# Optimization experiments

Measured on AMD Instinct MI355X. Metric: run time of the kernel, lower is better.

The kernel has to match this reference:

```python
import jax, jax.numpy as jnp
import numpy as np

# irreps: node in/out = 32x0e + 16x1o (dim 80), sh = 1x0e + 1x1o (dim 4)
N_NODES, N_EDGES = 8000, 64000
NUM_BASIS, RAD_HIDDEN = 8, 64
WEIGHT_NUMEL = 2304  # 32*32 + 32*16 + 16*16 + 16*32
EPS = 1e-8
INV_SQRT3 = 1.0 / np.sqrt(3.0)
# e3nn path weights (normalization='component', path_normalization='element'):
# into 0e outputs: sqrt(ir.dim=1 / (32+16)); into 1o outputs: sqrt(3 / (32+16))
PW0 = float(np.sqrt(1.0 / 48.0))
PW1 = float(np.sqrt(3.0 / 48.0))


def setup_inputs() -> dict:
    key = jax.random.key(0)
    ks = jax.random.split(key, 10)
    node_features = jax.random.normal(ks[0], (N_NODES, 80), dtype=jnp.float32)
    edge_index = jax.random.randint(ks[1], (2, N_EDGES), 0, N_NODES, dtype=jnp.int64)
    edge_sh = jax.random.normal(ks[2], (N_EDGES, 4), dtype=jnp.float32)
    edge_radial_emb = jax.random.uniform(ks[3], (N_EDGES, NUM_BASIS), dtype=jnp.float32)
    # RadialMLP params (Linear 8->64, SiLU, Linear 64->2304)
    rW1 = jax.random.normal(ks[4], (NUM_BASIS, RAD_HIDDEN), dtype=jnp.float32) / np.sqrt(NUM_BASIS)
    rb1 = jnp.zeros((RAD_HIDDEN,), dtype=jnp.float32)
    rW2 = jax.random.normal(ks[5], (RAD_HIDDEN, WEIGHT_NUMEL), dtype=jnp.float32) / np.sqrt(RAD_HIDDEN)
    rb2 = jnp.zeros((WEIGHT_NUMEL,), dtype=jnp.float32)
    # o3.Linear weights (per-irrep mixing matrices, e3nn init ~ N(0,1))
    Wl0 = jax.random.normal(ks[6], (32, 32), dtype=jnp.float32)
    Wl1 = jax.random.normal(ks[7], (16, 16), dtype=jnp.float32)
    return {"node_features": node_features, "edge_index": edge_index,
            "edge_sh": edge_sh, "edge_radial_emb": edge_radial_emb,
            "rW1": rW1, "rb1": rb1, "rW2": rW2, "rb2": rb2,
            "Wl0": Wl0, "Wl1": Wl1}


def reference(node_features, edge_index, edge_sh, edge_radial_emb,
              rW1, rb1, rW2, rb2, Wl0, Wl1):
    N = node_features.shape[0]
    src, dst = edge_index[0], edge_index[1]
    # radial MLP -> per-edge tensor-product weights [E, 2304] (fp32 path)
    h = jax.nn.silu(edge_radial_emb @ rW1 + rb1)
    tpw = h @ rW2 + rb2
    E = tpw.shape[0]
    wA = tpw[:, :1024].reshape(E, 32, 32)      # 0e x 0e -> 0e
    wB = tpw[:, 1024:1536].reshape(E, 32, 16)  # 0e x 1o -> 1o
    wC = tpw[:, 1536:1792].reshape(E, 16, 16)  # 1o x 0e -> 1o
    wD = tpw[:, 1792:2304].reshape(E, 16, 32)  # 1o x 1o -> 0e
    # gather source node features
    xs = node_features[src, :32]                       # [E,32] scalars
    xv = node_features[src, 32:].reshape(E, 16, 3)     # [E,16,3] vectors
    sh0 = edge_sh[:, 0]                                # [E]
    shv = edge_sh[:, 1:4]                              # [E,3]
    # equivariant tensor product messages
    dotv = jnp.einsum('euk,ek->eu', xv, shv)           # 1o.1o -> 0e
    msg_s = PW0 * (jnp.einsum('euw,eu->ew', wA, xs * sh0[:, None])
                   + INV_SQRT3 * jnp.einsum('euw,eu->eu' if False else 'euw,eu->ew', wD, dotv))
    msg_v = (PW1 * INV_SQRT3) * (jnp.einsum('euw,eu,ek->ewk', wB, xs, shv)
                                 + jnp.einsum('euw,euk->ewk', wC, xv) * sh0[:, None, None])
    messages = jnp.concatenate([msg_s, msg_v.reshape(E, 48)], axis=-1)  # [E,80]
    # scatter-sum aggregation over destination nodes
    agg = jax.ops.segment_sum(messages, dst, num_segments=N)            # [N,80]
    # equivariant linear (per-irrep mixing, fan-in normalized)
    lin_s = (agg[:, :32] @ Wl0) / np.sqrt(32.0)
    lin_v = jnp.einsum('nuk,uv->nvk', agg[:, 32:].reshape(N, 16, 3), Wl1) / np.sqrt(16.0)
    # SafeNormActivation: silu on scalars, norm-gated silu on vectors
    act_s = jax.nn.silu(lin_s)
    norms = jnp.linalg.norm(lin_v, axis=-1, keepdims=True)   # [N,16,1]
    safe = jnp.maximum(norms, EPS)
    act_v = jnp.where(norms < EPS, 0.0, (lin_v / safe) * jax.nn.silu(norms))
    activated = jnp.concatenate([act_s, act_v.reshape(N, 48)], axis=-1)
    # skip connection (irreps_in == irreps_out -> identity skip)
    return node_features + activated
```

## Files before the change

kernel.cpp:

```cpp
#include <hip/hip_runtime.h>
#include <math.h>

#define N_NODES_C 8000
#define N_EDGES_C 64000

static constexpr float PW0_C     = 0.14433756729740646f;
static constexpr float C1_C      = 0.14433756729740643f;
static constexpr float PW0IS3_C  = 0.08333333333333333f;
static constexpr float RS32_C    = 0.17677669529663687f;

typedef __attribute__((ext_vector_type(8))) short short8;
typedef __attribute__((ext_vector_type(4))) float f32x4;

__device__ __forceinline__ float silu_f(float x) { return x / (1.0f + expf(-x)); }

__device__ __forceinline__ unsigned short f2bf(float x) {
    union { float f; unsigned u; } a; a.f = x;
    unsigned r = a.u + 0x7fffu + ((a.u >> 16) & 1u);
    return (unsigned short)(r >> 16);
}
__device__ __forceinline__ float bf2f(unsigned short x) {
    union { unsigned u; float f; } a; a.u = ((unsigned)x) << 16; return a.f;
}

__device__ __forceinline__ void stage16(const void* g, void* lds) {
    __builtin_amdgcn_global_load_lds(
        (const __attribute__((address_space(1))) void*)g,
        (__attribute__((address_space(3))) void*)lds, 16, 0, 0);
}

__global__ __launch_bounds__(256) void prep_kernel(
    const float* __restrict__ rW2, unsigned short* __restrict__ rW2T)
{
    const int idx = blockIdx.x * 256 + threadIdx.x;
    const int k = idx / 2304, col = idx % 2304;
    rW2T[(size_t)col * 64 + k] = f2bf(rW2[idx]);
}

__global__ __launch_bounds__(256, 2) void edge_kernel_mfma(
    const float* __restrict__ nf,
    const int*   __restrict__ ei,
    const float* __restrict__ sh,
    const float* __restrict__ emb,
    const float* __restrict__ rW1,
    const float* __restrict__ rb1,
    const unsigned short* __restrict__ rW2T,
    const float* __restrict__ rb2,
    float* __restrict__ agg)
{
    __shared__ float pool_f[8192];
    __shared__ float rb2_s[2304];
    __shared__ float rW1_s[512];
    __shared__ unsigned short xs_s[128][34];
    __shared__ unsigned short xv_s[128][50];
    __shared__ float dv_s[128][17];
    __shared__ float sh0_s[128];
    __shared__ float shv_s[128][3];
    __shared__ int   dst_s[128];

    char*  stg = (char*)pool_f;
    float (*msg)[84] = reinterpret_cast<float(*)[84]>(pool_f);

    const int t    = threadIdx.x;
    const int e0   = blockIdx.x * 128;
    const int lane = t & 63, wv = t >> 6;
    const int l15  = lane & 15, lk = lane >> 4;
    const int l7   = l15 & 7;

    #define STAGEPAIR(pp, b) {                                                    \
        const char* gsrc = (const char*)rW2T + (size_t)(pp) * 16384;              \
        _Pragma("unroll")                                                         \
        for (int j = 0; j < 4; j++) {                                             \
            const int p_ = j * 256 + t;                                           \
            const int pr = p_ >> 3;                                               \
            const int sl = (p_ & 7) ^ (pr & 7);                                   \
            stage16(gsrc + pr * 128 + (sl << 4), stg + (b) * 16384 + p_ * 16);    \
        }                                                                         \
    }

    STAGEPAIR(0, 0)
    if (t < 128) {
        const int eid = e0 + t;
        dst_s[t] = ei[N_EDGES_C + eid];
        const float4 s4 = *reinterpret_cast<const float4*>(sh + (size_t)eid * 4);
        sh0_s[t] = s4.x;
        shv_s[t][0] = s4.y; shv_s[t][1] = s4.z; shv_s[t][2] = s4.w;
    }
    {
        const int e = t >> 1, q = t & 1;
        const int src = ei[e0 + e];
        const float* p = nf + (size_t)src * 80 + q * 40;
        #pragma unroll
        for (int f4 = 0; f4 < 10; f4++) {
            const float4 v = *reinterpret_cast<const float4*>(p + f4 * 4);
            const int g = q * 40 + f4 * 4;
            const float vv[4] = {v.x, v.y, v.z, v.w};
            #pragma unroll
            for (int ii = 0; ii < 4; ii++) {
                const int gg = g + ii;
                if (gg < 32) xs_s[e][gg]      = f2bf(vv[ii]);
                else         xv_s[e][gg - 32] = f2bf(vv[ii]);
            }
        }
    }
    for (int i = t; i < 512;  i += 256) rW1_s[i] = rW1[i];
    for (int i = t; i < 2304; i += 256) rb2_s[i] = rb2[i];
    __syncthreads();

    {
        const int e = t >> 1, u0d = (t & 1) * 8;
        #pragma unroll
        for (int i = 0; i < 8; i++) {
            const int u = u0d + i;
            dv_s[e][u] = bf2f(xv_s[e][u*3+0]) * shv_s[e][0]
                       + bf2f(xv_s[e][u*3+1]) * shv_s[e][1]
                       + bf2f(xv_s[e][u*3+2]) * shv_s[e][2];
        }
    }
    const int eA = wv * 32 + l15;
    const int eB = eA + 16;
    short8 bfr[2][2];
    {
        float embA[8], embB[8];
        {
            const float* pa = emb + (size_t)(e0 + eA) * 8;
            const float* pb = emb + (size_t)(e0 + eB) * 8;
            const float4 a0 = *reinterpret_cast<const float4*>(pa);
            const float4 a1 = *reinterpret_cast<const float4*>(pa + 4);
            const float4 b0 = *reinterpret_cast<const float4*>(pb);
            const float4 b1 = *reinterpret_cast<const float4*>(pb + 4);
            embA[0]=a0.x; embA[1]=a0.y; embA[2]=a0.z; embA[3]=a0.w;
            embA[4]=a1.x; embA[5]=a1.y; embA[6]=a1.z; embA[7]=a1.w;
            embB[0]=b0.x; embB[1]=b0.y; embB[2]=b0.z; embB[3]=b0.w;
            embB[4]=b1.x; embB[5]=b1.y; embB[6]=b1.z; embB[7]=b1.w;
        }
        #pragma unroll
        for (int s = 0; s < 2; s++) {
            const int k0 = s * 32 + lk * 8;
            const float4 r0 = *reinterpret_cast<const float4*>(rb1 + k0);
            const float4 r1 = *reinterpret_cast<const float4*>(rb1 + k0 + 4);
            float preA[8] = {r0.x,r0.y,r0.z,r0.w, r1.x,r1.y,r1.z,r1.w};
            float preB[8] = {r0.x,r0.y,r0.z,r0.w, r1.x,r1.y,r1.z,r1.w};
            #pragma unroll
            for (int b = 0; b < 8; b++) {
                const float4 wa = *reinterpret_cast<const float4*>(&rW1_s[b * 64 + k0]);
                const float4 wb = *reinterpret_cast<const float4*>(&rW1_s[b * 64 + k0 + 4]);
                const float wv4[8] = {wa.x,wa.y,wa.z,wa.w, wb.x,wb.y,wb.z,wb.w};
                #pragma unroll
                for (int j = 0; j < 8; j++) {
                    preA[j] = fmaf(embA[b], wv4[j], preA[j]);
                    preB[j] = fmaf(embB[b], wv4[j], preB[j]);
                }
            }
            short8 hA, hBv;
            #pragma unroll
            for (int j = 0; j < 8; j++) {
                hA[j]  = (short)f2bf(silu_f(preA[j]));
                hBv[j] = (short)f2bf(silu_f(preB[j]));
            }
            bfr[0][s] = hA; bfr[1][s] = hBv;
        }
    }
    const float sh0A = sh0_s[eA], sh0B = sh0_s[eB];
    const float fAA  = PW0_C * sh0A, fAB = PW0_C * sh0B;
    __syncthreads();

    float sA0[2][4] = {{0,0,0,0},{0,0,0,0}}, sA1[2][4] = {{0,0,0,0},{0,0,0,0}};
    float sB0[4] = {0,0,0,0},                sB1[4] = {0,0,0,0};
    float sC0[3][4] = {{0,0,0,0},{0,0,0,0},{0,0,0,0}};
    float sC1[3][4] = {{0,0,0,0},{0,0,0,0},{0,0,0,0}};

    #define GEMM2(cc, a0, a1) {                                                   \
        const int cb_ = (cc) * 64;                                                \
        const char* sb_ = stg + (((cc) >> 1) & 1) * 16384 + ((cc) & 1) * 8192;    \
        _Pragma("unroll")                                                         \
        for (int m = 0; m < 4; m++) {                                             \
            const float4 rbv = *reinterpret_cast<const float4*>(                  \
                &rb2_s[cb_ + m * 16 + lk * 4]);                                   \
            a0[m][0] = rbv.x; a0[m][1] = rbv.y; a0[m][2] = rbv.z; a0[m][3] = rbv.w; \
            a1[m][0] = rbv.x; a1[m][1] = rbv.y; a1[m][2] = rbv.z; a1[m][3] = rbv.w; \
        }                                                                         \
        _Pragma("unroll")                                                         \
        for (int s = 0; s < 2; s++) {                                             \
            _Pragma("unroll")                                                     \
            for (int m = 0; m < 4; m++) {                                         \
                const short8 a_ = *reinterpret_cast<const short8*>(               \
                    sb_ + (m * 16 + l15) * 128 + (((s * 4 + lk) ^ l7) << 4));     \
                a0[m] = __builtin_amdgcn_mfma_f32_16x16x32_bf16(a_, bfr[0][s], a0[m], 0, 0, 0); \
                a1[m] = __builtin_amdgcn_mfma_f32_16x16x32_bf16(a_, bfr[1][s], a1[m], 0, 0, 0); \
            }                                                                     \
        } }

    #define EPI(cc, a0, a1) {                                                     \
        const int c_ = (cc);                                                      \
        if (c_ < 16) {                                                            \
            const float xA0 = bf2f(xs_s[eA][c_*2]) * fAA, xA1 = bf2f(xs_s[eA][c_*2+1]) * fAA; \
            const float xB0 = bf2f(xs_s[eB][c_*2]) * fAB, xB1 = bf2f(xs_s[eB][c_*2+1]) * fAB; \
            _Pragma("unroll")                                                     \
            for (int r = 0; r < 4; r++) {                                         \
                sA0[0][r] = fmaf(a0[0][r], xA0, fmaf(a0[2][r], xA1, sA0[0][r]));  \
                sA0[1][r] = fmaf(a0[1][r], xA0, fmaf(a0[3][r], xA1, sA0[1][r]));  \
                sA1[0][r] = fmaf(a1[0][r], xB0, fmaf(a1[2][r], xB1, sA1[0][r]));  \
                sA1[1][r] = fmaf(a1[1][r], xB0, fmaf(a1[3][r], xB1, sA1[1][r]));  \
            }                                                                     \
        } else if (c_ < 24) {                                                     \
            const int u0 = (c_ - 16) * 4;                                         \
            float xA[4], xB[4];                                                   \
            _Pragma("unroll")                                                     \
            for (int m = 0; m < 4; m++) { xA[m] = bf2f(xs_s[eA][u0+m]); xB[m] = bf2f(xs_s[eB][u0+m]); } \
            _Pragma("unroll")                                                     \
            for (int r = 0; r < 4; r++) {                                         \
                sB0[r] = fmaf(a0[0][r], xA[0], fmaf(a0[1][r], xA[1],              \
                          fmaf(a0[2][r], xA[2], fmaf(a0[3][r], xA[3], sB0[r])))); \
                sB1[r] = fmaf(a1[0][r], xB[0], fmaf(a1[1][r], xB[1],              \
                          fmaf(a1[2][r], xB[2], fmaf(a1[3][r], xB[3], sB1[r])))); \
            }                                                                     \
        } else if (c_ < 28) {                                                     \
            const int u0 = (c_ - 24) * 4;                                         \
            _Pragma("unroll")                                                     \
            for (int k = 0; k < 3; k++) {                                         \
                float xA[4], xB[4];                                               \
                _Pragma("unroll")                                                 \
                for (int m = 0; m < 4; m++) {                                     \
                    xA[m] = bf2f(xv_s[eA][(u0+m)*3+k]);                           \
                    xB[m] = bf2f(xv_s[eB][(u0+m)*3+k]);                           \
                }                                                                 \
                _Pragma("unroll")                                                 \
                for (int r = 0; r < 4; r++) {                                     \
                    sC0[k][r] = fmaf(a0[0][r], xA[0], fmaf(a0[1][r], xA[1],       \
                                 fmaf(a0[2][r], xA[2], fmaf(a0[3][r], xA[3], sC0[k][r])))); \
                    sC1[k][r] = fmaf(a1[0][r], xB[0], fmaf(a1[1][r], xB[1],       \
                                 fmaf(a1[2][r], xB[2], fmaf(a1[3][r], xB[3], sC1[k][r])))); \
                }                                                                 \
            }                                                                     \
        } else {                                                                  \
            const int u0 = (c_ - 28) * 2;                                         \
            const float dA0 = dv_s[eA][u0] * PW0IS3_C, dA1 = dv_s[eA][u0+1] * PW0IS3_C; \
            const float dB0 = dv_s[eB][u0] * PW0IS3_C, dB1 = dv_s[eB][u0+1] * PW0IS3_C; \
            _Pragma("unroll")                                                     \
            for (int r = 0; r < 4; r++) {                                         \
                sA0[0][r] = fmaf(a0[0][r], dA0, fmaf(a0[2][r], dA1, sA0[0][r]));  \
                sA0[1][r] = fmaf(a0[1][r], dA0, fmaf(a0[3][r], dA1, sA0[1][r]));  \
                sA1[0][r] = fmaf(a1[0][r], dB0, fmaf(a1[2][r], dB1, sA1[0][r]));  \
                sA1[1][r] = fmaf(a1[1][r], dB0, fmaf(a1[3][r], dB1, sA1[1][r]));  \
            }                                                                     \
        } }

    f32x4 pA[4], pB[4], qA[4], qB[4];
    for (int p = 0; p < 18; ++p) {
        __builtin_amdgcn_s_barrier();
        if (p < 17) {
            STAGEPAIR(p + 1, (p + 1) & 1)
            asm volatile("s_waitcnt vmcnt(4)" ::: "memory");
        } else {
            asm volatile("s_waitcnt vmcnt(0)" ::: "memory");
        }
        __builtin_amdgcn_sched_barrier(0);
        const int c0 = 2 * p, c1 = 2 * p + 1;
        GEMM2(c0, pA, pB)
        GEMM2(c1, qA, qB)
        EPI(c0, pA, pB)
        EPI(c1, qA, qB)
    }
    #undef GEMM2
    #undef EPI
    #undef STAGEPAIR

    #pragma unroll
    for (int pass = 0; pass < 2; ++pass) {
        __syncthreads();
        if ((wv >> 1) == pass) {
            const int lr0 = (wv & 1) * 32 + l15;
            const int lr1 = lr0 + 16;
            #pragma unroll
            for (int hi = 0; hi < 2; hi++)
                #pragma unroll
                for (int r = 0; r < 4; r++) {
                    msg[lr0][hi * 16 + lk * 4 + r] = sA0[hi][r];
                    msg[lr1][hi * 16 + lk * 4 + r] = sA1[hi][r];
                }
            #pragma unroll
            for (int r = 0; r < 4; r++) {
                const int w = lk * 4 + r;
                #pragma unroll
                for (int k = 0; k < 3; k++) {
                    msg[lr0][32 + w * 3 + k] = C1_C * (sB0[r] * shv_s[eA][k] + sh0A * sC0[k][r]);
                    msg[lr1][32 + w * 3 + k] = C1_C * (sB1[r] * shv_s[eB][k] + sh0B * sC1[k][r]);
                }
            }
        }
        __syncthreads();
        const int ebase = pass * 64;
        for (int i = t; i < 64 * 80; i += 256) {
            const int rr = i / 80, m = i - rr * 80;
            atomicAdd(&agg[(size_t)dst_s[ebase + rr] * 80 + m], msg[rr][m]);
        }
    }
}

__global__ __launch_bounds__(256, 1) void edge_kernel_f32(
    const float* __restrict__ nf, const int* __restrict__ ei,
    const float* __restrict__ sh, const float* __restrict__ emb,
    const float* __restrict__ rW1, const float* __restrict__ rb1,
    const float* __restrict__ rW2, const float* __restrict__ rb2,
    float* __restrict__ agg)
{
    __shared__ float hT[64][68];
    __shared__ float tpw[64][132];
    __shared__ float xs_s[64][32];
    __shared__ float xv_s[64][48];
    __shared__ float dv_s[64][16];
    __shared__ float sh0_s[64];
    __shared__ float shv_s[64][3];
    __shared__ int   dst_s[64];
    __shared__ float msg[64][84];

    const int t  = threadIdx.x;
    const int e0 = blockIdx.x * 64;
    if (t < 64) {
        const int eid = e0 + t;
        dst_s[t] = ei[N_EDGES_C + eid];
        const float4 s4 = *reinterpret_cast<const float4*>(sh + (size_t)eid * 4);
        sh0_s[t] = s4.x; shv_s[t][0] = s4.y; shv_s[t][1] = s4.z; shv_s[t][2] = s4.w;
    }
    for (int i = t; i < 64 * 84; i += 256) (&msg[0][0])[i] = 0.0f;
    {
        const int e = t >> 2, q = t & 3;
        const int src = ei[e0 + e];
        const float* p = nf + (size_t)src * 80 + q * 20;
        #pragma unroll
        for (int f4 = 0; f4 < 5; f4++) {
            const float4 v = *reinterpret_cast<const float4*>(p + f4 * 4);
            const int g = q * 20 + f4 * 4;
            const float vv[4] = {v.x, v.y, v.z, v.w};
            #pragma unroll
            for (int ii = 0; ii < 4; ii++) {
                const int gg = g + ii;
                if (gg < 32) xs_s[e][gg] = vv[ii]; else xv_s[e][gg - 32] = vv[ii];
            }
        }
    }
    {
        const int c = t & 63, eg = t >> 6;
        float w1[8];
        #pragma unroll
        for (int b = 0; b < 8; b++) w1[b] = rW1[b * 64 + c];
        const float bias = rb1[c];
        #pragma unroll
        for (int rep = 0; rep < 16; rep++) {
            const int e = rep * 4 + eg;
            const float* em = emb + (size_t)(e0 + e) * 8;
            float pre = bias;
            #pragma unroll
            for (int b = 0; b < 8; b++) pre = fmaf(em[b], w1[b], pre);
            hT[c][e] = silu_f(pre);
        }
    }
    __syncthreads();
    {
        const int e = t >> 2, q = t & 3;
        #pragma unroll
        for (int i = 0; i < 4; i++) {
            const int u = q * 4 + i;
            dv_s[e][u] = xv_s[e][u*3+0]*shv_s[e][0] + xv_s[e][u*3+1]*shv_s[e][1]
                       + xv_s[e][u*3+2]*shv_s[e][2];
        }
    }
    __syncthreads();
    const int lane = t & 63, wv = t >> 6;
    for (int ch = 0; ch < 18; ch++) {
        const int jb = ch * 128;
        float acc[16][2];
        #pragma unroll
        for (int i = 0; i < 16; i++) { acc[i][0] = 0.0f; acc[i][1] = 0.0f; }
        const float* Bp = rW2 + jb + lane * 2;
        #pragma unroll 2
        for (int c = 0; c < 64; c++) {
            const float2 b = *reinterpret_cast<const float2*>(Bp + (size_t)c * 2304);
            const float4* ap = reinterpret_cast<const float4*>(&hT[c][wv * 16]);
            const float4 a0 = ap[0], a1 = ap[1], a2 = ap[2], a3 = ap[3];
            const float va[16] = {a0.x,a0.y,a0.z,a0.w, a1.x,a1.y,a1.z,a1.w,
                                  a2.x,a2.y,a2.z,a2.w, a3.x,a3.y,a3.z,a3.w};
            #pragma unroll
            for (int i = 0; i < 16; i++) {
                acc[i][0] = fmaf(va[i], b.x, acc[i][0]);
                acc[i][1] = fmaf(va[i], b.y, acc[i][1]);
            }
        }
        const float2 rb = *reinterpret_cast<const float2*>(rb2 + jb + lane * 2);
        __syncthreads();
        #pragma unroll
        for (int i = 0; i < 16; i++)
            *reinterpret_cast<float2*>(&tpw[wv * 16 + i][lane * 2]) =
                make_float2(acc[i][0] + rb.x, acc[i][1] + rb.y);
        __syncthreads();
        if (ch < 8) {
            const int u0 = ch * 4, w = t & 31, eg = t >> 5;
            #pragma unroll
            for (int ee = 0; ee < 8; ee++) {
                const int e = eg * 8 + ee;
                float s = 0.0f;
                #pragma unroll
                for (int du = 0; du < 4; du++) s = fmaf(tpw[e][du * 32 + w], xs_s[e][u0 + du], s);
                msg[e][w] = fmaf(PW0_C * sh0_s[e], s, msg[e][w]);
            }
        } else if (ch < 12) {
            const int u0 = (ch - 8) * 8, w = t & 15, eg = t >> 4;
            #pragma unroll
            for (int ee = 0; ee < 4; ee++) {
                const int e = eg * 4 + ee;
                float s = 0.0f;
                #pragma unroll
                for (int du = 0; du < 8; du++) s = fmaf(tpw[e][du * 16 + w], xs_s[e][u0 + du], s);
                const float c1s = C1_C * s;
                msg[e][32 + w*3 + 0] = fmaf(c1s, shv_s[e][0], msg[e][32 + w*3 + 0]);
                msg[e][32 + w*3 + 1] = fmaf(c1s, shv_s[e][1], msg[e][32 + w*3 + 1]);
                msg[e][32 + w*3 + 2] = fmaf(c1s, shv_s[e][2], msg[e][32 + w*3 + 2]);
            }
        } else if (ch < 14) {
            const int u0 = (ch - 12) * 8, w = t & 15, eg = t >> 4;
            #pragma unroll
            for (int ee = 0; ee < 4; ee++) {
                const int e = eg * 4 + ee;
                float s0 = 0, s1 = 0, s2 = 0;
                #pragma unroll
                for (int du = 0; du < 8; du++) {
                    const float tv = tpw[e][du * 16 + w];
                    const int u = u0 + du;
                    s0 = fmaf(tv, xv_s[e][u*3 + 0], s0);
                    s1 = fmaf(tv, xv_s[e][u*3 + 1], s1);
                    s2 = fmaf(tv, xv_s[e][u*3 + 2], s2);
                }
                const float f = C1_C * sh0_s[e];
                msg[e][32 + w*3 + 0] = fmaf(f, s0, msg[e][32 + w*3 + 0]);
                msg[e][32 + w*3 + 1] = fmaf(f, s1, msg[e][32 + w*3 + 1]);
                msg[e][32 + w*3 + 2] = fmaf(f, s2, msg[e][32 + w*3 + 2]);
            }
        } else {
            const int u0 = (ch - 14) * 4, w = t & 31, eg = t >> 5;
            #pragma unroll
            for (int ee = 0; ee < 8; ee++) {
                const int e = eg * 8 + ee;
                float s = 0.0f;
                #pragma unroll
                for (int du = 0; du < 4; du++) s = fmaf(tpw[e][du * 32 + w], dv_s[e][u0 + du], s);
                msg[e][w] = fmaf(PW0IS3_C, s, msg[e][w]);
            }
        }
    }
    __syncthreads();
    for (int i = t; i < 64 * 80; i += 256) {
        const int e = i / 80, m = i - e * 80;
        atomicAdd(&agg[(size_t)dst_s[e] * 80 + m], msg[e][m]);
    }
}

__global__ __launch_bounds__(256, 4) void node_kernel(
    const float* __restrict__ nf,
    float* __restrict__ io,
    const float* __restrict__ Wl0,
    const float* __restrict__ Wl1)
{
    __shared__ float a_s[4][80];
    const int t  = threadIdx.x;
    const int nb = blockIdx.x * 4;
    for (int i = t; i < 320; i += 256)
        a_s[i / 80][i % 80] = io[(size_t)nb * 80 + i];
    __syncthreads();

    const int ln = t >> 6;
    const int r  = t & 63;
    const int n  = nb + ln;
    const float* a = a_s[ln];
    if (r < 32) {
        float s = 0.0f;
        #pragma unroll
        for (int u = 0; u < 32; u++) s = fmaf(a[u], Wl0[u * 32 + r], s);
        s *= RS32_C;
        io[(size_t)n * 80 + r] = nf[(size_t)n * 80 + r] + silu_f(s);
    } else if (r < 48) {
        const int v = r - 32;
        float l0 = 0, l1 = 0, l2 = 0;
        #pragma unroll
        for (int u = 0; u < 16; u++) {
            const float w = Wl1[u * 16 + v];
            l0 = fmaf(a[32 + u*3 + 0], w, l0);
            l1 = fmaf(a[32 + u*3 + 1], w, l1);
            l2 = fmaf(a[32 + u*3 + 2], w, l2);
        }
        l0 *= 0.25f; l1 *= 0.25f; l2 *= 0.25f;
        const float norm = sqrtf(l0*l0 + l1*l1 + l2*l2);
        float f = 0.0f;
        if (norm >= 1e-8f) f = silu_f(norm) / norm;
        const size_t o = (size_t)n * 80 + 32 + (size_t)v * 3;
        io[o + 0] = nf[o + 0] + f * l0;
        io[o + 1] = nf[o + 1] + f * l1;
        io[o + 2] = nf[o + 2] + f * l2;
    }
}

extern "C" void kernel_launch(void* const* d_in, const int* in_sizes, int n_in,
                              void* d_out, int out_size, void* d_ws, size_t ws_size,
                              hipStream_t stream) {
    const float* nf  = (const float*)d_in[0];
    const int*   ei  = (const int*)d_in[1];
    const float* sh  = (const float*)d_in[2];
    const float* emb = (const float*)d_in[3];
    const float* rW1 = (const float*)d_in[4];
    const float* rb1 = (const float*)d_in[5];
    const float* rW2 = (const float*)d_in[6];
    const float* rb2 = (const float*)d_in[7];
    const float* Wl0 = (const float*)d_in[8];
    const float* Wl1 = (const float*)d_in[9];

    float* agg = (float*)d_out;
    hipMemsetAsync(agg, 0, (size_t)N_NODES_C * 80 * sizeof(float), stream);

    const size_t rW2T_bytes = (size_t)2304 * 64 * sizeof(unsigned short);
    if (d_ws != nullptr && ws_size >= rW2T_bytes) {
        unsigned short* rW2T = (unsigned short*)d_ws;
        prep_kernel<<<(2304 * 64) / 256, 256, 0, stream>>>(rW2, rW2T);
        edge_kernel_mfma<<<N_EDGES_C / 128, 256, 0, stream>>>(
            nf, ei, sh, emb, rW1, rb1, rW2T, rb2, agg);
    } else {
        edge_kernel_f32<<<N_EDGES_C / 64, 256, 0, stream>>>(
            nf, ei, sh, emb, rW1, rb1, rW2, rb2, agg);
    }
    node_kernel<<<N_NODES_C / 4, 256, 0, stream>>>(nf, agg, Wl0, Wl1);
}
```

Before: 64.24 us.

## Replace scatter atomics with per-node edge lists and gather in node kernel

The edge kernel now records each edge in a per-destination bucket list, using an atomic counter with a fixed max degree. Each message is written to a dense per-edge buffer instead of atomically added into the aggregate; edges that overflow a bucket still fall back to atomics. A new node kernel gathers the listed messages per node, adds them to the atomic residue, and applies the linear mixing and activation. This trades about 5M float atomics for one int atomic per edge, plus a 20MB message buffer write and a gathered read.

```diff
diff --git a/kernel.cpp b/kernel.cpp
--- a/kernel.cpp
+++ b/kernel.cpp
@@ -3,6 +3,7 @@
 
 #define N_NODES_C 8000
 #define N_EDGES_C 64000
+#define MAXDEG_C  64
 
 static constexpr float PW0_C     = 0.14433756729740646f;
 static constexpr float C1_C      = 0.14433756729740643f;
@@ -46,7 +47,11 @@
     const float* __restrict__ rb1,
     const unsigned short* __restrict__ rW2T,
     const float* __restrict__ rb2,
-    float* __restrict__ agg)
+    float* __restrict__ agg,
+    float* __restrict__ msgbuf,
+    int*   __restrict__ cnt,
+    int*   __restrict__ list,
+    const int use_ws)
 {
     __shared__ float pool_f[8192];
     __shared__ float rb2_s[2304];
@@ -57,6 +62,7 @@
     __shared__ float sh0_s[128];
     __shared__ float shv_s[128][3];
     __shared__ int   dst_s[128];
+    __shared__ int   slot_s[128];
 
     char*  stg = (char*)pool_f;
     float (*msg)[84] = reinterpret_cast<float(*)[84]>(pool_f);
@@ -81,10 +87,16 @@
     STAGEPAIR(0, 0)
     if (t < 128) {
         const int eid = e0 + t;
-        dst_s[t] = ei[N_EDGES_C + eid];
+        const int d = ei[N_EDGES_C + eid];
+        dst_s[t] = d;
         const float4 s4 = *reinterpret_cast<const float4*>(sh + (size_t)eid * 4);
         sh0_s[t] = s4.x;
         shv_s[t][0] = s4.y; shv_s[t][1] = s4.z; shv_s[t][2] = s4.w;
+        if (use_ws) {
+            const int s = atomicAdd(&cnt[d], 1);
+            slot_s[t] = s;
+            if (s < MAXDEG_C) list[d * MAXDEG_C + s] = eid;
+        }
     }
     {
         const int e = t >> 1, q = t & 1;
@@ -291,10 +303,81 @@
         }
         __syncthreads();
         const int ebase = pass * 64;
-        for (int i = t; i < 64 * 80; i += 256) {
-            const int rr = i / 80, m = i - rr * 80;
-            atomicAdd(&agg[(size_t)dst_s[ebase + rr] * 80 + m], msg[rr][m]);
-        }
+        if (use_ws) {
+            for (int i = t; i < 64 * 80; i += 256) {
+                const int rr = i / 80, m = i - rr * 80;
+                const int eg = ebase + rr;
+                if (slot_s[eg] < MAXDEG_C)
+                    msgbuf[(size_t)(e0 + eg) * 80 + m] = msg[rr][m];
+                else
+                    atomicAdd(&agg[(size_t)dst_s[eg] * 80 + m], msg[rr][m]);
+            }
+        } else {
+            for (int i = t; i < 64 * 80; i += 256) {
+                const int rr = i / 80, m = i - rr * 80;
+                atomicAdd(&agg[(size_t)dst_s[ebase + rr] * 80 + m], msg[rr][m]);
+            }
+        }
+    }
+}
+
+__global__ __launch_bounds__(256, 4) void node_kernel2(
+    const float* __restrict__ nf,
+    float* __restrict__ io,
+    const float* __restrict__ Wl0,
+    const float* __restrict__ Wl1,
+    const float* __restrict__ msgbuf,
+    const int*   __restrict__ cnt,
+    const int*   __restrict__ list)
+{
+    __shared__ float a_s[16][81];
+    const int t  = threadIdx.x;
+    const int ln = t >> 4, j = t & 15;
+    const int n  = blockIdx.x * 16 + ln;
+
+    float acc[5];
+    #pragma unroll
+    for (int q = 0; q < 5; q++) acc[q] = io[(size_t)n * 80 + j + 16 * q];
+    const int deg = cnt[n];
+    const int dl  = deg < MAXDEG_C ? deg : MAXDEG_C;
+    for (int d = 0; d < dl; ++d) {
+        const int eid = list[n * MAXDEG_C + d];
+        const float* mrow = msgbuf + (size_t)eid * 80;
+        #pragma unroll
+        for (int q = 0; q < 5; q++) acc[q] += mrow[j + 16 * q];
+    }
+    #pragma unroll
+    for (int q = 0; q < 5; q++) a_s[ln][j + 16 * q] = acc[q];
+    __syncthreads();
+
+    const float* a = a_s[ln];
+    {
+        float s0 = 0, s1 = 0;
+        #pragma unroll
+        for (int u = 0; u < 32; u++) {
+            s0 = fmaf(a[u], Wl0[u * 32 + j],      s0);
+            s1 = fmaf(a[u], Wl0[u * 32 + j + 16], s1);
+        }
+        s0 *= RS32_C; s1 *= RS32_C;
+        io[(size_t)n * 80 + j]      = nf[(size_t)n * 80 + j]      + silu_f(s0);
+        io[(size_t)n * 80 + j + 16] = nf[(size_t)n * 80 + j + 16] + silu_f(s1);
+    }
+    {
+        float l0 = 0, l1 = 0, l2 = 0;
+        #pragma unroll
+        for (int u = 0; u < 16; u++) {
+            const float w = Wl1[u * 16 + j];
+            l0 = fmaf(a[32 + u*3 + 0], w, l0);
+            l1 = fmaf(a[32 + u*3 + 1], w, l1);
+            l2 = fmaf(a[32 + u*3 + 2], w, l2);
+        }
+        l0 *= 0.25f; l1 *= 0.25f; l2 *= 0.25f;
+        const float norm = sqrtf(l0*l0 + l1*l1 + l2*l2);
+        const float f = (norm >= 1e-8f) ? silu_f(norm) / norm : 0.0f;
+        const size_t o = (size_t)n * 80 + 32 + (size_t)j * 3;
+        io[o + 0] = nf[o + 0] + f * l0;
+        io[o + 1] = nf[o + 1] + f * l1;
+        io[o + 2] = nf[o + 2] + f * l2;
     }
 }
 
@@ -517,14 +600,33 @@
     hipMemsetAsync(agg, 0, (size_t)N_NODES_C * 80 * sizeof(float), stream);
 
     const size_t rW2T_bytes = (size_t)2304 * 64 * sizeof(unsigned short);
+    const size_t OFF_CNT  = (size_t)512 << 10;
+    const size_t OFF_LIST = (size_t)1 << 20;
+    const size_t OFF_MSG  = (size_t)4 << 20;
+    const size_t need_big = OFF_MSG + (size_t)N_EDGES_C * 80 * sizeof(float);
+
     if (d_ws != nullptr && ws_size >= rW2T_bytes) {
         unsigned short* rW2T = (unsigned short*)d_ws;
         prep_kernel<<<(2304 * 64) / 256, 256, 0, stream>>>(rW2, rW2T);
+
+        const int use_ws = (ws_size >= need_big) ? 1 : 0;
+        float* msgbuf = (float*)((char*)d_ws + OFF_MSG);
+        int*   cnt    = (int*)((char*)d_ws + OFF_CNT);
+        int*   list   = (int*)((char*)d_ws + OFF_LIST);
+        if (use_ws)
+            hipMemsetAsync(cnt, 0, (size_t)N_NODES_C * sizeof(int), stream);
+
         edge_kernel_mfma<<<N_EDGES_C / 128, 256, 0, stream>>>(
-            nf, ei, sh, emb, rW1, rb1, rW2T, rb2, agg);
+            nf, ei, sh, emb, rW1, rb1, rW2T, rb2, agg, msgbuf, cnt, list, use_ws);
+
+        if (use_ws)
+            node_kernel2<<<N_NODES_C / 16, 256, 0, stream>>>(
+                nf, agg, Wl0, Wl1, msgbuf, cnt, list);
+        else
+            node_kernel<<<N_NODES_C / 4, 256, 0, stream>>>(nf, agg, Wl0, Wl1);
     } else {
         edge_kernel_f32<<<N_EDGES_C / 64, 256, 0, stream>>>(
             nf, ei, sh, emb, rW1, rb1, rW2, rb2, agg);
-    }
-    node_kernel<<<N_NODES_C / 4, 256, 0, stream>>>(nf, agg, Wl0, Wl1);
-}
+        node_kernel<<<N_NODES_C / 4, 256, 0, stream>>>(nf, agg, Wl0, Wl1);
+    }
+}
```

New measurement: 74.86 us. 16.5% more time.

## Cut LDS use for three blocks per CU with triple-buffered single-chunk staging

Applied to the files above, without the earlier changes.

Shrinks shared memory by dropping the rW1/rb2 LDS copies (read from global instead), storing dv as bf16, and replacing the double-buffered chunk-pair staging with a triple-buffered ring of single 8KB chunks. Launch bounds are raised to 3 blocks per CU so more waves can hide latency. Each loop iteration now processes one chunk with one accumulator set, which lowers register pressure but adds a barrier per chunk and more global bias loads. The bf16 rounding of dv adds a small precision loss.

```diff
diff --git a/kernel.cpp b/kernel.cpp
--- a/kernel.cpp
+++ b/kernel.cpp
@@ -37,7 +37,7 @@
     rW2T[(size_t)col * 64 + k] = f2bf(rW2[idx]);
 }
 
-__global__ __launch_bounds__(256, 2) void edge_kernel_mfma(
+__global__ __launch_bounds__(256, 3) void edge_kernel_mfma(
     const float* __restrict__ nf,
     const int*   __restrict__ ei,
     const float* __restrict__ sh,
@@ -48,12 +48,10 @@
     const float* __restrict__ rb2,
     float* __restrict__ agg)
 {
-    __shared__ float pool_f[8192];
-    __shared__ float rb2_s[2304];
-    __shared__ float rW1_s[512];
+    __shared__ float pool_f[6144];
     __shared__ unsigned short xs_s[128][34];
     __shared__ unsigned short xv_s[128][50];
-    __shared__ float dv_s[128][17];
+    __shared__ unsigned short dv_s[128][18];
     __shared__ float sh0_s[128];
     __shared__ float shv_s[128][3];
     __shared__ int   dst_s[128];
@@ -67,18 +65,19 @@
     const int l15  = lane & 15, lk = lane >> 4;
     const int l7   = l15 & 7;
 
-    #define STAGEPAIR(pp, b) {                                                    \
-        const char* gsrc = (const char*)rW2T + (size_t)(pp) * 16384;              \
+    #define STAGE(cc, b) {                                                        \
+        const char* gsrc = (const char*)rW2T + (size_t)(cc) * 8192;               \
         _Pragma("unroll")                                                         \
-        for (int j = 0; j < 4; j++) {                                             \
+        for (int j = 0; j < 2; j++) {                                             \
             const int p_ = j * 256 + t;                                           \
             const int pr = p_ >> 3;                                               \
             const int sl = (p_ & 7) ^ (pr & 7);                                   \
-            stage16(gsrc + pr * 128 + (sl << 4), stg + (b) * 16384 + p_ * 16);    \
+            stage16(gsrc + pr * 128 + (sl << 4), stg + (b) * 8192 + p_ * 16);     \
         }                                                                         \
     }
 
-    STAGEPAIR(0, 0)
+    STAGE(0, 0)
+    STAGE(1, 1)
     if (t < 128) {
         const int eid = e0 + t;
         dst_s[t] = ei[N_EDGES_C + eid];
@@ -103,8 +102,6 @@
             }
         }
     }
-    for (int i = t; i < 512;  i += 256) rW1_s[i] = rW1[i];
-    for (int i = t; i < 2304; i += 256) rb2_s[i] = rb2[i];
     __syncthreads();
 
     {
@@ -112,9 +109,10 @@
         #pragma unroll
         for (int i = 0; i < 8; i++) {
             const int u = u0d + i;
-            dv_s[e][u] = bf2f(xv_s[e][u*3+0]) * shv_s[e][0]
-                       + bf2f(xv_s[e][u*3+1]) * shv_s[e][1]
-                       + bf2f(xv_s[e][u*3+2]) * shv_s[e][2];
+            const float d = bf2f(xv_s[e][u*3+0]) * shv_s[e][0]
+                          + bf2f(xv_s[e][u*3+1]) * shv_s[e][1]
+                          + bf2f(xv_s[e][u*3+2]) * shv_s[e][2];
+            dv_s[e][u] = f2bf(d);
         }
     }
     const int eA = wv * 32 + l15;
@@ -143,8 +141,8 @@
             float preB[8] = {r0.x,r0.y,r0.z,r0.w, r1.x,r1.y,r1.z,r1.w};
             #pragma unroll
             for (int b = 0; b < 8; b++) {
-                const float4 wa = *reinterpret_cast<const float4*>(&rW1_s[b * 64 + k0]);
-                const float4 wb = *reinterpret_cast<const float4*>(&rW1_s[b * 64 + k0 + 4]);
+                const float4 wa = *reinterpret_cast<const float4*>(&rW1[b * 64 + k0]);
+                const float4 wb = *reinterpret_cast<const float4*>(&rW1[b * 64 + k0 + 4]);
                 const float wv4[8] = {wa.x,wa.y,wa.z,wa.w, wb.x,wb.y,wb.z,wb.w};
                 #pragma unroll
                 for (int j = 0; j < 8; j++) {
@@ -170,13 +168,13 @@
     float sC0[3][4] = {{0,0,0,0},{0,0,0,0},{0,0,0,0}};
     float sC1[3][4] = {{0,0,0,0},{0,0,0,0},{0,0,0,0}};
 
-    #define GEMM2(cc, a0, a1) {                                                   \
+    #define GEMM2(cc, bb, a0, a1) {                                              \
         const int cb_ = (cc) * 64;                                                \
-        const char* sb_ = stg + (((cc) >> 1) & 1) * 16384 + ((cc) & 1) * 8192;    \
+        const char* sb_ = stg + (bb) * 8192;                                      \
         _Pragma("unroll")                                                         \
         for (int m = 0; m < 4; m++) {                                             \
             const float4 rbv = *reinterpret_cast<const float4*>(                  \
-                &rb2_s[cb_ + m * 16 + lk * 4]);                                   \
+                rb2 + cb_ + m * 16 + lk * 4);                                     \
             a0[m][0] = rbv.x; a0[m][1] = rbv.y; a0[m][2] = rbv.z; a0[m][3] = rbv.w; \
             a1[m][0] = rbv.x; a1[m][1] = rbv.y; a1[m][2] = rbv.z; a1[m][3] = rbv.w; \
         }                                                                         \
@@ -235,8 +233,8 @@
             }                                                                     \
         } else {                                                                  \
             const int u0 = (c_ - 28) * 2;                                         \
-            const float dA0 = dv_s[eA][u0] * PW0IS3_C, dA1 = dv_s[eA][u0+1] * PW0IS3_C; \
-            const float dB0 = dv_s[eB][u0] * PW0IS3_C, dB1 = dv_s[eB][u0+1] * PW0IS3_C; \
+            const float dA0 = bf2f(dv_s[eA][u0]) * PW0IS3_C, dA1 = bf2f(dv_s[eA][u0+1]) * PW0IS3_C; \
+            const float dB0 = bf2f(dv_s[eB][u0]) * PW0IS3_C, dB1 = bf2f(dv_s[eB][u0+1]) * PW0IS3_C; \
             _Pragma("unroll")                                                     \
             for (int r = 0; r < 4; r++) {                                         \
                 sA0[0][r] = fmaf(a0[0][r], dA0, fmaf(a0[2][r], dA1, sA0[0][r]));  \
@@ -246,25 +244,27 @@
             }                                                                     \
         } }
 
-    f32x4 pA[4], pB[4], qA[4], qB[4];
-    for (int p = 0; p < 18; ++p) {
+    f32x4 pA[4], pB[4];
+    int b2 = 2;
+    for (int c = 0; c < 36; ++c) {
         __builtin_amdgcn_s_barrier();
-        if (p < 17) {
-            STAGEPAIR(p + 1, (p + 1) & 1)
+        if (c < 34) {
+            STAGE(c + 2, b2)
             asm volatile("s_waitcnt vmcnt(4)" ::: "memory");
+        } else if (c == 34) {
+            asm volatile("s_waitcnt vmcnt(2)" ::: "memory");
         } else {
             asm volatile("s_waitcnt vmcnt(0)" ::: "memory");
         }
         __builtin_amdgcn_sched_barrier(0);
-        const int c0 = 2 * p, c1 = 2 * p + 1;
-        GEMM2(c0, pA, pB)
-        GEMM2(c1, qA, qB)
-        EPI(c0, pA, pB)
-        EPI(c1, qA, qB)
+        const int bc = (b2 + 1) % 3;
+        GEMM2(c, bc, pA, pB)
+        EPI(c, pA, pB)
+        b2 = bc;
     }
     #undef GEMM2
     #undef EPI
-    #undef STAGEPAIR
+    #undef STAGE
 
     #pragma unroll
     for (int pass = 0; pass < 2; ++pass) {
```

Result: slower. 73.37 us (+14.2%).

## Load radial weight fragments directly from global into registers instead of LDS staging

Applied to the files above, without the earlier changes.

Removes the double-buffered global-to-LDS staging of the bf16 rW2T weight tiles and their per-iteration barriers. Each wave now loads its MFMA A-fragments straight from global memory (served by L2/L1) into registers, with a two-deep register prefetch across column chunks. This drops the 32KB staging pool and barrier synchronisation, which may raise occupancy. The cost is that every wave fetches the same weights redundantly through the cache hierarchy, and register pressure goes up.

```diff
diff --git a/kernel.cpp b/kernel.cpp
--- a/kernel.cpp
+++ b/kernel.cpp
@@ -21,12 +21,6 @@
 }
 __device__ __forceinline__ float bf2f(unsigned short x) {
     union { unsigned u; float f; } a; a.u = ((unsigned)x) << 16; return a.f;
-}
-
-__device__ __forceinline__ void stage16(const void* g, void* lds) {
-    __builtin_amdgcn_global_load_lds(
-        (const __attribute__((address_space(1))) void*)g,
-        (__attribute__((address_space(3))) void*)lds, 16, 0, 0);
 }
 
 __global__ __launch_bounds__(256) void prep_kernel(
@@ -48,7 +42,6 @@
     const float* __restrict__ rb2,
     float* __restrict__ agg)
 {
-    __shared__ float pool_f[8192];
     __shared__ float rb2_s[2304];
     __shared__ float rW1_s[512];
     __shared__ unsigned short xs_s[128][34];
@@ -57,28 +50,13 @@
     __shared__ float sh0_s[128];
     __shared__ float shv_s[128][3];
     __shared__ int   dst_s[128];
-
-    char*  stg = (char*)pool_f;
-    float (*msg)[84] = reinterpret_cast<float(*)[84]>(pool_f);
+    __shared__ float msg[64][84];
 
     const int t    = threadIdx.x;
     const int e0   = blockIdx.x * 128;
     const int lane = t & 63, wv = t >> 6;
     const int l15  = lane & 15, lk = lane >> 4;
-    const int l7   = l15 & 7;
-
-    #define STAGEPAIR(pp, b) {                                                    \
-        const char* gsrc = (const char*)rW2T + (size_t)(pp) * 16384;              \
-        _Pragma("unroll")                                                         \
-        for (int j = 0; j < 4; j++) {                                             \
-            const int p_ = j * 256 + t;                                           \
-            const int pr = p_ >> 3;                                               \
-            const int sl = (p_ & 7) ^ (pr & 7);                                   \
-            stage16(gsrc + pr * 128 + (sl << 4), stg + (b) * 16384 + p_ * 16);    \
-        }                                                                         \
-    }
-
-    STAGEPAIR(0, 0)
+
     if (t < 128) {
         const int eid = e0 + t;
         dst_s[t] = ei[N_EDGES_C + eid];
@@ -170,9 +148,18 @@
     float sC0[3][4] = {{0,0,0,0},{0,0,0,0},{0,0,0,0}};
     float sC1[3][4] = {{0,0,0,0},{0,0,0,0},{0,0,0,0}};
 
-    #define GEMM2(cc, a0, a1) {                                                   \
+    #define LOADA(cc, dst) {                                                      \
         const int cb_ = (cc) * 64;                                                \
-        const char* sb_ = stg + (((cc) >> 1) & 1) * 16384 + ((cc) & 1) * 8192;    \
+        _Pragma("unroll")                                                         \
+        for (int s = 0; s < 2; s++)                                               \
+            _Pragma("unroll")                                                     \
+            for (int m = 0; m < 4; m++)                                           \
+                dst[s * 4 + m] = *reinterpret_cast<const short8*>(                \
+                    rW2T + (size_t)(cb_ + m * 16 + l15) * 64 + s * 32 + lk * 8);  \
+    }
+
+    #define GEMMR(cc, af, a0, a1) {                                               \
+        const int cb_ = (cc) * 64;                                                \
         _Pragma("unroll")                                                         \
         for (int m = 0; m < 4; m++) {                                             \
             const float4 rbv = *reinterpret_cast<const float4*>(                  \
@@ -184,10 +171,8 @@
         for (int s = 0; s < 2; s++) {                                             \
             _Pragma("unroll")                                                     \
             for (int m = 0; m < 4; m++) {                                         \
-                const short8 a_ = *reinterpret_cast<const short8*>(               \
-                    sb_ + (m * 16 + l15) * 128 + (((s * 4 + lk) ^ l7) << 4));     \
-                a0[m] = __builtin_amdgcn_mfma_f32_16x16x32_bf16(a_, bfr[0][s], a0[m], 0, 0, 0); \
-                a1[m] = __builtin_amdgcn_mfma_f32_16x16x32_bf16(a_, bfr[1][s], a1[m], 0, 0, 0); \
+                a0[m] = __builtin_amdgcn_mfma_f32_16x16x32_bf16(af[s*4+m], bfr[0][s], a0[m], 0, 0, 0); \
+                a1[m] = __builtin_amdgcn_mfma_f32_16x16x32_bf16(af[s*4+m], bfr[1][s], a1[m], 0, 0, 0); \
             }                                                                     \
         } }
 
@@ -246,25 +231,25 @@
             }                                                                     \
         } }
 
-    f32x4 pA[4], pB[4], qA[4], qB[4];
-    for (int p = 0; p < 18; ++p) {
-        __builtin_amdgcn_s_barrier();
-        if (p < 17) {
-            STAGEPAIR(p + 1, (p + 1) & 1)
-            asm volatile("s_waitcnt vmcnt(4)" ::: "memory");
-        } else {
-            asm volatile("s_waitcnt vmcnt(0)" ::: "memory");
-        }
-        __builtin_amdgcn_sched_barrier(0);
-        const int c0 = 2 * p, c1 = 2 * p + 1;
-        GEMM2(c0, pA, pB)
-        GEMM2(c1, qA, qB)
-        EPI(c0, pA, pB)
-        EPI(c1, qA, qB)
-    }
-    #undef GEMM2
+    short8 afA[8], afB[8];
+    LOADA(0, afA)
+    for (int c = 0; c < 36; c += 2) {
+        if (c + 1 < 36) LOADA(c + 1, afB)
+        {
+            f32x4 a0[4], a1[4];
+            GEMMR(c, afA, a0, a1)
+            EPI(c, a0, a1)
+        }
+        if (c + 2 < 36) LOADA(c + 2, afA)
+        {
+            f32x4 a0[4], a1[4];
+            GEMMR(c + 1, afB, a0, a1)
+            EPI(c + 1, a0, a1)
+        }
+    }
+    #undef LOADA
+    #undef GEMMR
     #undef EPI
-    #undef STAGEPAIR
 
     #pragma unroll
     for (int pass = 0; pass < 2; ++pass) {
```

New measurement: 104.6 us. +62.8%, slower.
